# Kernel tuning notes

Measured on AMD Instinct MI355X. Metric: run time of the kernel, lower is better.

## Reference

```python
import jax, jax.numpy as jnp
from jax import lax
import numpy as np

# config constants (must match init_kwargs)
G = 64            # grid_size
N_CH = 16         # n_channels
HID = 128         # hidden_dim
N_FROZEN = 4
N_GROWN = 12
CH_EXIST = 0
CH_ANCH = 1
STREET = 3        # street_levels
UPDATE_SCALE = 0.1
B = 2


def _make_kernels():
    d = np.array([-1.0, 0.0, 1.0], np.float32)
    s = np.array([1.0, 2.0, 1.0], np.float32)
    sx = np.einsum('i,j,k->ijk', s, s, d) / 16.0
    sy = np.einsum('i,j,k->ijk', s, d, s) / 16.0
    sz = np.einsum('i,j,k->ijk', d, s, s) / 16.0
    ident = np.zeros((3, 3, 3), np.float32)
    ident[1, 1, 1] = 1.0
    return jnp.asarray(np.stack([ident, sx, sy, sz], axis=0))  # [4,3,3,3]

_KERNELS = _make_kernels()


def _perceive(x):
    # x: [B,C,D,H,W]; replicate-pad then 4 depthwise 3x3x3 stencils, concat k-major
    C = x.shape[1]
    xp = jnp.pad(x, ((0, 0), (0, 0), (1, 1), (1, 1), (1, 1)), mode='edge')
    outs = []
    for k in range(4):
        w = jnp.tile(_KERNELS[k][None, None], (C, 1, 1, 1, 1))  # [C,1,3,3,3]
        outs.append(lax.conv_general_dilated(
            xp, w, window_strides=(1, 1, 1), padding='VALID',
            dimension_numbers=('NCDHW', 'OIDHW', 'NCDHW'),
            feature_group_count=C))
    return jnp.concatenate(outs, axis=1)  # [B,4C,D,H,W]


def _pw(x, w, b):
    # 1x1x1 conv3d == per-voxel linear
    return jnp.einsum('bcdhw,oc->bodhw', x, w) + b[None, :, None, None, None]


def _legality_field(state):
    existing = state[:, CH_EXIST]   # [B,D,H,W]
    anchors = state[:, CH_ANCH]
    z = jnp.arange(G).reshape(1, G, 1, 1)
    above = (z >= STREET).astype(state.dtype)
    at = (z < STREET).astype(state.dtype)
    pos = above + at * anchors
    return jnp.clip((1.0 - existing) * pos, 0.0, 1.0)


def _step(state, w1, b1, w2, b2, w3, b3):
    perc = _perceive(state)
    h = jax.nn.relu(_pw(perc, w1, b1))
    h = jax.nn.relu(_pw(h, w2, b2))
    delta = _pw(h, w3, b3)  # [B,N_GROWN,D,H,W]  (eval mode: no fire mask)
    grown = jnp.clip(state[:, N_FROZEN:] + UPDATE_SCALE * delta, 0.0, 1.0)
    available = 1.0 - state[:, CH_EXIST:CH_EXIST + 1]
    struct = grown[:, 0:1] * available
    struct = struct * _legality_field(state)[:, None]
    grown_masked = jnp.concatenate([struct, grown[:, 1:]], axis=1)
    return jnp.concatenate([state[:, :N_FROZEN], grown_masked], axis=1)


def setup_inputs() -> dict:
    key = jax.random.key(0)
    ks = jax.random.split(key, 7)
    state = jax.random.uniform(ks[0], (B, N_CH, G, G, G), dtype=jnp.float32)
    w1 = jax.random.normal(ks[1], (HID, 4 * N_CH), dtype=jnp.float32) * 0.05
    b1 = jnp.zeros((HID,), jnp.float32)
    w2 = jax.random.normal(ks[2], (HID, HID), dtype=jnp.float32) * 0.05
    b2 = jnp.zeros((HID,), jnp.float32)
    w3 = jax.random.normal(ks[3], (N_GROWN, HID), dtype=jnp.float32) * 0.02
    b3 = jnp.zeros((N_GROWN,), jnp.float32)
    return {'state': state, 'w1': w1, 'b1': b1, 'w2': w2, 'b2': b2,
            'w3': w3, 'b3': b3, 'steps': 1}


def reference(state, w1, b1, w2, b2, w3, b3, steps):
    for _ in range(steps):
        state = _step(state, w1, b1, w2, b2, w3, b3)
    return state
```

## Files before the change

### kernel.cpp

```cpp
#include <hip/hip_runtime.h>


namespace {

using short8   = __attribute__((ext_vector_type(8))) short;
using ushort4v = __attribute__((ext_vector_type(4))) unsigned short;
using uint4v   = __attribute__((ext_vector_type(4))) unsigned int;
using float4v  = __attribute__((ext_vector_type(4))) float;

__device__ inline unsigned short f2bf(float x) {
    return (unsigned short)((__float_as_uint(x) + 0x8000u) >> 16);
}
__device__ inline unsigned pkbf(float lo, float hi) {
    const unsigned a = __float_as_uint(lo) + 0x8000u;
    const unsigned b = __float_as_uint(hi) + 0x8000u;
    return (a >> 16) | (b & 0xFFFF0000u);
}

__global__ void prep_weights(const float* __restrict__ w1,
                             const float* __restrict__ w2,
                             const float* __restrict__ w3,
                             unsigned short* __restrict__ wsb) {
    const int i = blockIdx.x * 256 + threadIdx.x;
    if (i < 128 * 64)  wsb[i] = f2bf(w1[i]);
    if (i < 128 * 128) wsb[8192 + i] = f2bf(w2[i]);
    if (i < 16 * 128)  wsb[24576 + i] = (i < 12 * 128) ? f2bf(w3[i])
                                                       : (unsigned short)0;
}

constexpr int PSTRIDE = 88;
constexpr int HSTRIDE = 152;
constexpr int LDS_US  = 4 * 64 * HSTRIDE;
static_assert(256 * PSTRIDE <= LDS_US, "P must fit under H");

__global__ __launch_bounds__(256, 2)
void nca_mfma(const float* __restrict__ state,
              const float* __restrict__ b1, const float* __restrict__ b2,
              const float* __restrict__ b3,
              const unsigned short* __restrict__ wsb,
              float* __restrict__ out) {
    __shared__ unsigned short ldsH[LDS_US];

    const unsigned short* w1b = wsb;
    const unsigned short* w2b = wsb + 8192;
    const unsigned short* w3b = wsb + 24576;

    const int tid  = threadIdx.x;
    const int lane = tid & 63;
    const int wv   = tid >> 6;
    const int gv0  = blockIdx.x * 256;

    const int gvp = gv0 + tid;
    const int y = (gvp >> 6) & 63;
    const int z = (gvp >> 12) & 63;
    const int b = gvp >> 18;
    const long bbase = (long)b << 22;
    const int vox = gvp & 262143;

    {
        const int x = lane;
        const int zc[3] = {(z > 0 ? z - 1 : 0) << 12, z << 12,
                           (z < 63 ? z + 1 : 63) << 12};
        const int yc[3] = {(y > 0 ? y - 1 : 0) << 6, y << 6,
                           (y < 63 ? y + 1 : 63) << 6};
        int roff[9];
        #pragma unroll
        for (int i = 0; i < 3; ++i)
            #pragma unroll
            for (int j = 0; j < 3; ++j)
                roff[i * 3 + j] = zc[i] + yc[j] + x;

        const int lm = (lane > 0) ? lane - 1 : 0;
        const int lp = (lane < 63) ? lane + 1 : 63;

        unsigned pid[8], psx[8], psy[8], psz[8];
        float eid = 0.f, esx = 0.f, esy = 0.f, esz = 0.f;

        #pragma unroll
        for (int c = 0; c < 16; ++c) {
            const float* p = state + bbase + ((long)c << 18);
            float v[9];
            #pragma unroll
            for (int k = 0; k < 9; ++k) v[k] = p[roff[k]];

            const float ry0 = v[0] + 2.f * v[1] + v[2];
            const float ry1 = v[3] + 2.f * v[4] + v[5];
            const float ry2 = v[6] + 2.f * v[7] + v[8];
            const float A  = ry0 + 2.f * ry1 + ry2;
            const float By = (v[2] - v[0]) + 2.f * (v[5] - v[3])
                           + (v[8] - v[6]);
            const float Bz = (v[6] - v[0]) + 2.f * (v[7] - v[1])
                           + (v[8] - v[2]);

            const float Am  = __shfl(A,  lm, 64), Ap  = __shfl(A,  lp, 64);
            const float Bym = __shfl(By, lm, 64), Byp = __shfl(By, lp, 64);
            const float Bzm = __shfl(Bz, lm, 64), Bzp = __shfl(Bz, lp, 64);

            const float ident = v[4];
            const float sx = (Ap - Am) * 0.0625f;
            const float sy = (Bym + Byp + 2.f * By) * 0.0625f;
            const float sz = (Bzm + Bzp + 2.f * Bz) * 0.0625f;

            if (c < 4)
                out[bbase + ((long)c << 18) + vox] = ident;

            if (c & 1) {
                pid[c >> 1] = pkbf(eid, ident);
                psx[c >> 1] = pkbf(esx, sx);
                psy[c >> 1] = pkbf(esy, sy);
                psz[c >> 1] = pkbf(esz, sz);
            } else {
                eid = ident; esx = sx; esy = sy; esz = sz;
            }
        }

        unsigned short* Pr = ldsH + tid * PSTRIDE;
        *(uint4v*)&Pr[0]  = uint4v{pid[0], pid[1], pid[2], pid[3]};
        *(uint4v*)&Pr[8]  = uint4v{pid[4], pid[5], pid[6], pid[7]};
        *(uint4v*)&Pr[16] = uint4v{psx[0], psx[1], psx[2], psx[3]};
        *(uint4v*)&Pr[24] = uint4v{psx[4], psx[5], psx[6], psx[7]};
        *(uint4v*)&Pr[32] = uint4v{psy[0], psy[1], psy[2], psy[3]};
        *(uint4v*)&Pr[40] = uint4v{psy[4], psy[5], psy[6], psy[7]};
        *(uint4v*)&Pr[48] = uint4v{psz[0], psz[1], psz[2], psz[3]};
        *(uint4v*)&Pr[56] = uint4v{psz[4], psz[5], psz[6], psz[7]};
    }
    __syncthreads();

    const int n16  = lane & 15;
    const int quad = lane >> 4;
    unsigned short* Hw = ldsH + wv * 64 * HSTRIDE;

    float4v acc[8][4];

    #pragma unroll
    for (int rt = 0; rt < 8; ++rt)
        #pragma unroll
        for (int reg = 0; reg < 4; ++reg) {
            const float bb = b1[rt * 16 + quad * 4 + reg];
            #pragma unroll
            for (int nt = 0; nt < 4; ++nt) acc[rt][nt][reg] = bb;
        }

    short8 bP[4][2];
    #pragma unroll
    for (int nt = 0; nt < 4; ++nt)
        #pragma unroll
        for (int ks = 0; ks < 2; ++ks)
            bP[nt][ks] = *(const short8*)&ldsH[(wv * 64 + nt * 16 + n16) * PSTRIDE
                                               + ks * 32 + quad * 8];
    #pragma unroll
    for (int rt = 0; rt < 8; ++rt)
        #pragma unroll
        for (int ks = 0; ks < 2; ++ks) {
            const short8 a = *(const short8*)&w1b[(rt * 16 + n16) * 64
                                                   + ks * 32 + quad * 8];
            #pragma unroll
            for (int nt = 0; nt < 4; ++nt)
                acc[rt][nt] = __builtin_amdgcn_mfma_f32_16x16x32_bf16(
                    a, bP[nt][ks], acc[rt][nt], 0, 0, 0);
        }

    __syncthreads();

    #pragma unroll
    for (int rt = 0; rt < 8; ++rt)
        #pragma unroll
        for (int nt = 0; nt < 4; ++nt) {
            ushort4v hp;
            #pragma unroll
            for (int reg = 0; reg < 4; ++reg)
                hp[reg] = f2bf(fmaxf(acc[rt][nt][reg], 0.f));
            *(ushort4v*)&Hw[(nt * 16 + n16) * HSTRIDE + rt * 16 + quad * 4] = hp;
        }

    #pragma unroll
    for (int rt = 0; rt < 8; ++rt)
        #pragma unroll
        for (int reg = 0; reg < 4; ++reg) {
            const float bb = b2[rt * 16 + quad * 4 + reg];
            #pragma unroll
            for (int nt = 0; nt < 4; ++nt) acc[rt][nt][reg] = bb;
        }
    #pragma unroll
    for (int s = 0; s < 4; ++s) {
        short8 bh[4];
        #pragma unroll
        for (int nt = 0; nt < 4; ++nt)
            bh[nt] = *(const short8*)&Hw[(nt * 16 + n16) * HSTRIDE
                                          + s * 32 + quad * 8];
        #pragma unroll
        for (int rt = 0; rt < 8; ++rt) {
            const short8 a = *(const short8*)&w2b[(rt * 16 + n16) * 128
                                                   + s * 32 + quad * 8];
            #pragma unroll
            for (int nt = 0; nt < 4; ++nt)
                acc[rt][nt] = __builtin_amdgcn_mfma_f32_16x16x32_bf16(
                    a, bh[nt], acc[rt][nt], 0, 0, 0);
        }
    }

    #pragma unroll
    for (int rt = 0; rt < 8; ++rt)
        #pragma unroll
        for (int nt = 0; nt < 4; ++nt) {
            ushort4v hp;
            #pragma unroll
            for (int reg = 0; reg < 4; ++reg)
                hp[reg] = f2bf(fmaxf(acc[rt][nt][reg], 0.f));
            *(ushort4v*)&Hw[(nt * 16 + n16) * HSTRIDE + rt * 16 + quad * 4] = hp;
        }

    float4v acc3[4];
    #pragma unroll
    for (int reg = 0; reg < 4; ++reg) {
        const int rr = quad * 4 + reg;
        const float bb = (rr < 12) ? b3[rr] : 0.f;
        #pragma unroll
        for (int nt = 0; nt < 4; ++nt) acc3[nt][reg] = bb;
    }
    #pragma unroll
    for (int s = 0; s < 4; ++s) {
        const short8 a = *(const short8*)&w3b[n16 * 128 + s * 32 + quad * 8];
        #pragma unroll
        for (int nt = 0; nt < 4; ++nt) {
            const short8 bh = *(const short8*)&Hw[(nt * 16 + n16) * HSTRIDE
                                                   + s * 32 + quad * 8];
            acc3[nt] = __builtin_amdgcn_mfma_f32_16x16x32_bf16(
                a, bh, acc3[nt], 0, 0, 0);
        }
    }

    #pragma unroll
    for (int nt = 0; nt < 4; ++nt) {
        const int gv = gv0 + wv * 64 + nt * 16 + n16;
        const int vx = gv & 262143;
        const int zz = (gv >> 12) & 63;

        const float s0 = state[bbase + vx];
        const float s1 = state[bbase + (1 << 18) + vx];
        const float avail = 1.f - s0;
        const float pos = (zz >= 3) ? 1.f : s1;
        const float legal = fminf(fmaxf(avail * pos, 0.f), 1.f);

        #pragma unroll
        for (int reg = 0; reg < 4; ++reg) {
            const int rr = quad * 4 + reg;
            if (rr < 12) {
                const long off = bbase + ((long)(4 + rr) << 18) + vx;
                const float cen = state[off];
                float g = cen + 0.1f * acc3[nt][reg];
                g = fminf(fmaxf(g, 0.f), 1.f);
                if (rr == 0) g = g * avail * legal;
                out[off] = g;
            }
        }
    }
}

}

extern "C" void kernel_launch(void* const* d_in, const int* in_sizes, int n_in,
                              void* d_out, int out_size, void* d_ws, size_t ws_size,
                              hipStream_t stream) {
    const float* state = (const float*)d_in[0];
    const float* w1    = (const float*)d_in[1];
    const float* b1    = (const float*)d_in[2];
    const float* w2    = (const float*)d_in[3];
    const float* b2    = (const float*)d_in[4];
    const float* w3    = (const float*)d_in[5];
    const float* b3    = (const float*)d_in[6];
    float* out = (float*)d_out;
    unsigned short* wsb = (unsigned short*)d_ws;

    prep_weights<<<dim3(64), dim3(256), 0, stream>>>(w1, w2, w3, wsb);

    const int total = 2 * 64 * 64 * 64;
    nca_mfma<<<dim3(total / 256), dim3(256), 0, stream>>>(
        state, b1, b2, b3, wsb, out);
}
```

Before: 169.1 us.

## Keep hidden activations in registers via permuted weights, drop LDS round-trips

Reorders the K dimension of w2 and w3 at prep time so that the MFMA accumulator layout of one layer can be repacked directly into B-operand registers for the next layer. This removes the LDS write and read of the hidden activations and the block barriers. The perception tile is stored in a smaller XOR-swizzled LDS buffer, and each wave processes its 64 voxels in two halves to cut register pressure. Occupancy is raised to 4 blocks per CU. The risks are register spills and reloading the weights twice, once per half.

```diff
diff --git a/kernel.cpp b/kernel.cpp
--- a/kernel.cpp
+++ b/kernel.cpp
@@ -4,7 +4,6 @@
 namespace {
 
 using short8   = __attribute__((ext_vector_type(8))) short;
-using ushort4v = __attribute__((ext_vector_type(4))) unsigned short;
 using uint4v   = __attribute__((ext_vector_type(4))) unsigned int;
 using float4v  = __attribute__((ext_vector_type(4))) float;
 
@@ -15,6 +14,9 @@
     const unsigned a = __float_as_uint(lo) + 0x8000u;
     const unsigned b = __float_as_uint(hi) + 0x8000u;
     return (a >> 16) | (b & 0xFFFF0000u);
+}
+__device__ inline int pik(int k) {
+    return (k & 0xE0) | (((k >> 3) & 3) << 2) | (((k >> 2) & 1) << 4) | (k & 3);
 }
 
 __global__ void prep_weights(const float* __restrict__ w1,
@@ -23,23 +25,24 @@
                              unsigned short* __restrict__ wsb) {
     const int i = blockIdx.x * 256 + threadIdx.x;
     if (i < 128 * 64)  wsb[i] = f2bf(w1[i]);
-    if (i < 128 * 128) wsb[8192 + i] = f2bf(w2[i]);
-    if (i < 16 * 128)  wsb[24576 + i] = (i < 12 * 128) ? f2bf(w3[i])
-                                                       : (unsigned short)0;
-}
-
-constexpr int PSTRIDE = 88;
-constexpr int HSTRIDE = 152;
-constexpr int LDS_US  = 4 * 64 * HSTRIDE;
-static_assert(256 * PSTRIDE <= LDS_US, "P must fit under H");
-
-__global__ __launch_bounds__(256, 2)
+    if (i < 128 * 128) {
+        const int r = i >> 7, k = i & 127;
+        wsb[8192 + i] = f2bf(w2[r * 128 + pik(k)]);
+    }
+    if (i < 16 * 128) {
+        const int r = i >> 7, k = i & 127;
+        wsb[24576 + i] = (r < 12) ? f2bf(w3[r * 128 + pik(k)])
+                                  : (unsigned short)0;
+    }
+}
+
+__global__ __launch_bounds__(256, 4)
 void nca_mfma(const float* __restrict__ state,
               const float* __restrict__ b1, const float* __restrict__ b2,
               const float* __restrict__ b3,
               const unsigned short* __restrict__ wsb,
               float* __restrict__ out) {
-    __shared__ unsigned short ldsH[LDS_US];
+    __shared__ unsigned short ldsP[256 * 64];
 
     const unsigned short* w1b = wsb;
     const unsigned short* w2b = wsb + 8192;
@@ -48,17 +51,14 @@
     const int tid  = threadIdx.x;
     const int lane = tid & 63;
     const int wv   = tid >> 6;
-    const int gv0  = blockIdx.x * 256;
-
-    const int gvp = gv0 + tid;
-    const int y = (gvp >> 6) & 63;
-    const int z = (gvp >> 12) & 63;
-    const int b = gvp >> 18;
-    const long bbase = (long)b << 22;
-    const int vox = gvp & 262143;
+
+    const int wrow   = blockIdx.x * 4 + wv;
+    const int y      = wrow & 63;
+    const int z      = (wrow >> 6) & 63;
+    const long bbase = (long)(wrow >> 12) << 22;
+    const int rowvox = (wrow & 4095) << 6;
 
     {
-        const int x = lane;
         const int zc[3] = {(z > 0 ? z - 1 : 0) << 12, z << 12,
                            (z < 63 ? z + 1 : 63) << 12};
         const int yc[3] = {(y > 0 ? y - 1 : 0) << 6, y << 6,
@@ -68,7 +68,7 @@
         for (int i = 0; i < 3; ++i)
             #pragma unroll
             for (int j = 0; j < 3; ++j)
-                roff[i * 3 + j] = zc[i] + yc[j] + x;
+                roff[i * 3 + j] = zc[i] + yc[j] + lane;
 
         const int lm = (lane > 0) ? lane - 1 : 0;
         const int lp = (lane < 63) ? lane + 1 : 63;
@@ -102,7 +102,7 @@
             const float sz = (Bzm + Bzp + 2.f * Bz) * 0.0625f;
 
             if (c < 4)
-                out[bbase + ((long)c << 18) + vox] = ident;
+                out[bbase + ((long)c << 18) + rowvox + lane] = ident;
 
             if (c & 1) {
                 pid[c >> 1] = pkbf(eid, ident);
@@ -114,144 +114,132 @@
             }
         }
 
-        unsigned short* Pr = ldsH + tid * PSTRIDE;
-        *(uint4v*)&Pr[0]  = uint4v{pid[0], pid[1], pid[2], pid[3]};
-        *(uint4v*)&Pr[8]  = uint4v{pid[4], pid[5], pid[6], pid[7]};
-        *(uint4v*)&Pr[16] = uint4v{psx[0], psx[1], psx[2], psx[3]};
-        *(uint4v*)&Pr[24] = uint4v{psx[4], psx[5], psx[6], psx[7]};
-        *(uint4v*)&Pr[32] = uint4v{psy[0], psy[1], psy[2], psy[3]};
-        *(uint4v*)&Pr[40] = uint4v{psy[4], psy[5], psy[6], psy[7]};
-        *(uint4v*)&Pr[48] = uint4v{psz[0], psz[1], psz[2], psz[3]};
-        *(uint4v*)&Pr[56] = uint4v{psz[4], psz[5], psz[6], psz[7]};
-    }
-    __syncthreads();
+        unsigned short* Pr = ldsP + tid * 64;
+        const int sw = tid & 7;
+        *(uint4v*)&Pr[(0 ^ sw) << 3] = uint4v{pid[0], pid[1], pid[2], pid[3]};
+        *(uint4v*)&Pr[(1 ^ sw) << 3] = uint4v{pid[4], pid[5], pid[6], pid[7]};
+        *(uint4v*)&Pr[(2 ^ sw) << 3] = uint4v{psx[0], psx[1], psx[2], psx[3]};
+        *(uint4v*)&Pr[(3 ^ sw) << 3] = uint4v{psx[4], psx[5], psx[6], psx[7]};
+        *(uint4v*)&Pr[(4 ^ sw) << 3] = uint4v{psy[0], psy[1], psy[2], psy[3]};
+        *(uint4v*)&Pr[(5 ^ sw) << 3] = uint4v{psy[4], psy[5], psy[6], psy[7]};
+        *(uint4v*)&Pr[(6 ^ sw) << 3] = uint4v{psz[0], psz[1], psz[2], psz[3]};
+        *(uint4v*)&Pr[(7 ^ sw) << 3] = uint4v{psz[4], psz[5], psz[6], psz[7]};
+    }
 
     const int n16  = lane & 15;
     const int quad = lane >> 4;
-    unsigned short* Hw = ldsH + wv * 64 * HSTRIDE;
-
-    float4v acc[8][4];
-
-    #pragma unroll
-    for (int rt = 0; rt < 8; ++rt)
-        #pragma unroll
-        for (int reg = 0; reg < 4; ++reg) {
-            const float bb = b1[rt * 16 + quad * 4 + reg];
-            #pragma unroll
-            for (int nt = 0; nt < 4; ++nt) acc[rt][nt][reg] = bb;
-        }
-
-    short8 bP[4][2];
-    #pragma unroll
-    for (int nt = 0; nt < 4; ++nt)
-        #pragma unroll
-        for (int ks = 0; ks < 2; ++ks)
-            bP[nt][ks] = *(const short8*)&ldsH[(wv * 64 + nt * 16 + n16) * PSTRIDE
-                                               + ks * 32 + quad * 8];
-    #pragma unroll
-    for (int rt = 0; rt < 8; ++rt)
+    const unsigned short* Pw = ldsP + wv * (64 * 64);
+    const int psw = n16 & 7;
+
+    for (int half = 0; half < 2; ++half) {
+        float4v acc[8][2];
+        #pragma unroll
+        for (int rt = 0; rt < 8; ++rt)
+            #pragma unroll
+            for (int reg = 0; reg < 4; ++reg) {
+                const float bb = b1[rt * 16 + quad * 4 + reg];
+                acc[rt][0][reg] = bb;
+                acc[rt][1][reg] = bb;
+            }
+
         #pragma unroll
         for (int ks = 0; ks < 2; ++ks) {
-            const short8 a = *(const short8*)&w1b[(rt * 16 + n16) * 64
-                                                   + ks * 32 + quad * 8];
-            #pragma unroll
-            for (int nt = 0; nt < 4; ++nt)
-                acc[rt][nt] = __builtin_amdgcn_mfma_f32_16x16x32_bf16(
-                    a, bP[nt][ks], acc[rt][nt], 0, 0, 0);
-        }
-
-    __syncthreads();
-
-    #pragma unroll
-    for (int rt = 0; rt < 8; ++rt)
-        #pragma unroll
-        for (int nt = 0; nt < 4; ++nt) {
-            ushort4v hp;
-            #pragma unroll
-            for (int reg = 0; reg < 4; ++reg)
-                hp[reg] = f2bf(fmaxf(acc[rt][nt][reg], 0.f));
-            *(ushort4v*)&Hw[(nt * 16 + n16) * HSTRIDE + rt * 16 + quad * 4] = hp;
-        }
-
-    #pragma unroll
-    for (int rt = 0; rt < 8; ++rt)
-        #pragma unroll
-        for (int reg = 0; reg < 4; ++reg) {
-            const float bb = b2[rt * 16 + quad * 4 + reg];
-            #pragma unroll
-            for (int nt = 0; nt < 4; ++nt) acc[rt][nt][reg] = bb;
-        }
-    #pragma unroll
-    for (int s = 0; s < 4; ++s) {
-        short8 bh[4];
-        #pragma unroll
-        for (int nt = 0; nt < 4; ++nt)
-            bh[nt] = *(const short8*)&Hw[(nt * 16 + n16) * HSTRIDE
-                                          + s * 32 + quad * 8];
-        #pragma unroll
-        for (int rt = 0; rt < 8; ++rt) {
-            const short8 a = *(const short8*)&w2b[(rt * 16 + n16) * 128
-                                                   + s * 32 + quad * 8];
-            #pragma unroll
-            for (int nt = 0; nt < 4; ++nt)
-                acc[rt][nt] = __builtin_amdgcn_mfma_f32_16x16x32_bf16(
-                    a, bh[nt], acc[rt][nt], 0, 0, 0);
-        }
-    }
-
-    #pragma unroll
-    for (int rt = 0; rt < 8; ++rt)
-        #pragma unroll
-        for (int nt = 0; nt < 4; ++nt) {
-            ushort4v hp;
-            #pragma unroll
-            for (int reg = 0; reg < 4; ++reg)
-                hp[reg] = f2bf(fmaxf(acc[rt][nt][reg], 0.f));
-            *(ushort4v*)&Hw[(nt * 16 + n16) * HSTRIDE + rt * 16 + quad * 4] = hp;
-        }
-
-    float4v acc3[4];
-    #pragma unroll
-    for (int reg = 0; reg < 4; ++reg) {
-        const int rr = quad * 4 + reg;
-        const float bb = (rr < 12) ? b3[rr] : 0.f;
-        #pragma unroll
-        for (int nt = 0; nt < 4; ++nt) acc3[nt][reg] = bb;
-    }
-    #pragma unroll
-    for (int s = 0; s < 4; ++s) {
-        const short8 a = *(const short8*)&w3b[n16 * 128 + s * 32 + quad * 8];
-        #pragma unroll
-        for (int nt = 0; nt < 4; ++nt) {
-            const short8 bh = *(const short8*)&Hw[(nt * 16 + n16) * HSTRIDE
-                                                   + s * 32 + quad * 8];
-            acc3[nt] = __builtin_amdgcn_mfma_f32_16x16x32_bf16(
-                a, bh, acc3[nt], 0, 0, 0);
-        }
-    }
-
-    #pragma unroll
-    for (int nt = 0; nt < 4; ++nt) {
-        const int gv = gv0 + wv * 64 + nt * 16 + n16;
-        const int vx = gv & 262143;
-        const int zz = (gv >> 12) & 63;
-
-        const float s0 = state[bbase + vx];
-        const float s1 = state[bbase + (1 << 18) + vx];
-        const float avail = 1.f - s0;
-        const float pos = (zz >= 3) ? 1.f : s1;
-        const float legal = fminf(fmaxf(avail * pos, 0.f), 1.f);
-
+            const int ch = ((ks * 4 + quad) ^ psw) << 3;
+            const short8 bP0 = *(const short8*)
+                &Pw[((half * 2 + 0) * 16 + n16) * 64 + ch];
+            const short8 bP1 = *(const short8*)
+                &Pw[((half * 2 + 1) * 16 + n16) * 64 + ch];
+            #pragma unroll
+            for (int rt = 0; rt < 8; ++rt) {
+                const short8 a = *(const short8*)&w1b[(rt * 16 + n16) * 64
+                                                       + ks * 32 + quad * 8];
+                acc[rt][0] = __builtin_amdgcn_mfma_f32_16x16x32_bf16(
+                    a, bP0, acc[rt][0], 0, 0, 0);
+                acc[rt][1] = __builtin_amdgcn_mfma_f32_16x16x32_bf16(
+                    a, bP1, acc[rt][1], 0, 0, 0);
+            }
+        }
+
+        uint4v hq[2][4];
+        #pragma unroll
+        for (int i = 0; i < 2; ++i)
+            #pragma unroll
+            for (int sp = 0; sp < 4; ++sp)
+                hq[i][sp] = uint4v{
+                    pkbf(fmaxf(acc[2*sp  ][i][0], 0.f), fmaxf(acc[2*sp  ][i][1], 0.f)),
+                    pkbf(fmaxf(acc[2*sp  ][i][2], 0.f), fmaxf(acc[2*sp  ][i][3], 0.f)),
+                    pkbf(fmaxf(acc[2*sp+1][i][0], 0.f), fmaxf(acc[2*sp+1][i][1], 0.f)),
+                    pkbf(fmaxf(acc[2*sp+1][i][2], 0.f), fmaxf(acc[2*sp+1][i][3], 0.f))};
+
+        #pragma unroll
+        for (int rt = 0; rt < 8; ++rt)
+            #pragma unroll
+            for (int reg = 0; reg < 4; ++reg) {
+                const float bb = b2[rt * 16 + quad * 4 + reg];
+                acc[rt][0][reg] = bb;
+                acc[rt][1][reg] = bb;
+            }
+        #pragma unroll
+        for (int s = 0; s < 4; ++s) {
+            const short8 bh0 = __builtin_bit_cast(short8, hq[0][s]);
+            const short8 bh1 = __builtin_bit_cast(short8, hq[1][s]);
+            #pragma unroll
+            for (int rt = 0; rt < 8; ++rt) {
+                const short8 a = *(const short8*)&w2b[(rt * 16 + n16) * 128
+                                                       + s * 32 + quad * 8];
+                acc[rt][0] = __builtin_amdgcn_mfma_f32_16x16x32_bf16(
+                    a, bh0, acc[rt][0], 0, 0, 0);
+                acc[rt][1] = __builtin_amdgcn_mfma_f32_16x16x32_bf16(
+                    a, bh1, acc[rt][1], 0, 0, 0);
+            }
+        }
+
+        #pragma unroll
+        for (int i = 0; i < 2; ++i)
+            #pragma unroll
+            for (int sp = 0; sp < 4; ++sp)
+                hq[i][sp] = uint4v{
+                    pkbf(fmaxf(acc[2*sp  ][i][0], 0.f), fmaxf(acc[2*sp  ][i][1], 0.f)),
+                    pkbf(fmaxf(acc[2*sp  ][i][2], 0.f), fmaxf(acc[2*sp  ][i][3], 0.f)),
+                    pkbf(fmaxf(acc[2*sp+1][i][0], 0.f), fmaxf(acc[2*sp+1][i][1], 0.f)),
+                    pkbf(fmaxf(acc[2*sp+1][i][2], 0.f), fmaxf(acc[2*sp+1][i][3], 0.f))};
+
+        float4v acc3[2];
         #pragma unroll
         for (int reg = 0; reg < 4; ++reg) {
             const int rr = quad * 4 + reg;
-            if (rr < 12) {
-                const long off = bbase + ((long)(4 + rr) << 18) + vx;
-                const float cen = state[off];
-                float g = cen + 0.1f * acc3[nt][reg];
-                g = fminf(fmaxf(g, 0.f), 1.f);
-                if (rr == 0) g = g * avail * legal;
-                out[off] = g;
+            const float bb = (rr < 12) ? b3[rr] : 0.f;
+            acc3[0][reg] = bb;
+            acc3[1][reg] = bb;
+        }
+        #pragma unroll
+        for (int s = 0; s < 4; ++s) {
+            const short8 a = *(const short8*)&w3b[n16 * 128 + s * 32 + quad * 8];
+            acc3[0] = __builtin_amdgcn_mfma_f32_16x16x32_bf16(
+                a, __builtin_bit_cast(short8, hq[0][s]), acc3[0], 0, 0, 0);
+            acc3[1] = __builtin_amdgcn_mfma_f32_16x16x32_bf16(
+                a, __builtin_bit_cast(short8, hq[1][s]), acc3[1], 0, 0, 0);
+        }
+
+        #pragma unroll
+        for (int i = 0; i < 2; ++i) {
+            const int vx = rowvox + (half * 2 + i) * 16 + n16;
+            const float s0 = state[bbase + vx];
+            const float s1 = state[bbase + (1 << 18) + vx];
+            const float avail = 1.f - s0;
+            const float pos = (z >= 3) ? 1.f : s1;
+            const float legal = fminf(fmaxf(avail * pos, 0.f), 1.f);
+
+            #pragma unroll
+            for (int reg = 0; reg < 4; ++reg) {
+                const int rr = quad * 4 + reg;
+                if (rr < 12) {
+                    const long off = bbase + ((long)(4 + rr) << 18) + vx;
+                    float g = state[off] + 0.1f * acc3[i][reg];
+                    g = fminf(fmaxf(g, 0.f), 1.f);
+                    if (rr == 0) g = g * avail * legal;
+                    out[off] = g;
+                }
             }
         }
     }
```

New measurement: 511.6 us. 202% more time.
